# Optimization experiments

Hardware: AMD Instinct MI355X
Metric: run time of the kernel (lower is better)

## Reference

```python
import jax, jax.numpy as jnp
import numpy as np

DIM = 1024
HEADS = 16
HEAD_DIM = DIM // HEADS
MLP_HIDDEN = 4 * DIM
OUT_DIM = 1000
V_DIM = 1024
EPS = 1e-5
SCALE = DIM ** -0.5  # note: module scales by hidden_dim**-0.5, not head_dim**-0.5


def layer_norm(x, g, b):
    mu = jnp.mean(x, axis=-1, keepdims=True)
    var = jnp.mean(jnp.square(x - mu), axis=-1, keepdims=True)
    return (x - mu) * jax.lax.rsqrt(var + EPS) * g + b


def setup_inputs() -> dict:
    key = jax.random.key(0)
    ks = jax.random.split(key, 12)
    B, N = 4, 2048
    s = lambda fan_in: 1.0 / np.sqrt(fan_in)
    return {
        "x": jax.random.normal(ks[0], (B, N, DIM), jnp.float32),
        "value": jax.random.normal(ks[1], (B, N, V_DIM), jnp.float32),
        "wq": jax.random.normal(ks[2], (DIM, DIM), jnp.float32) * s(DIM),
        "wk": jax.random.normal(ks[3], (DIM, DIM), jnp.float32) * s(DIM),
        "wv": jax.random.normal(ks[4], (V_DIM, DIM), jnp.float32) * s(V_DIM),
        "w_ap": jax.random.normal(ks[5], (DIM, DIM), jnp.float32) * s(DIM),
        "b_ap": jnp.zeros((DIM,), jnp.float32),
        "g1": jnp.ones((DIM,), jnp.float32),
        "be1": jnp.zeros((DIM,), jnp.float32),
        "g2": jnp.ones((DIM,), jnp.float32),
        "be2": jnp.zeros((DIM,), jnp.float32),
        "w1": jax.random.normal(ks[6], (DIM, MLP_HIDDEN), jnp.float32) * s(DIM),
        "b1": jnp.zeros((MLP_HIDDEN,), jnp.float32),
        "w2": jax.random.normal(ks[7], (MLP_HIDDEN, DIM), jnp.float32) * s(MLP_HIDDEN),
        "b2": jnp.zeros((DIM,), jnp.float32),
        "w_out": jax.random.normal(ks[8], (DIM, OUT_DIM), jnp.float32) * s(DIM),
        "b_out": jnp.zeros((OUT_DIM,), jnp.float32),
    }


def reference(x, value, wq, wk, wv, w_ap, b_ap, g1, be1, g2, be2, w1, b1, w2, b2, w_out, b_out):
    B, N, C = x.shape
    xn = layer_norm(x, g1, be1)                      # [B,N,C]
    q = (xn @ wq).reshape(B, N, HEADS, HEAD_DIM)     # query and key both from norm1(x)
    k = (xn @ wk).reshape(B, N, HEADS, HEAD_DIM)
    v = (value @ wv).reshape(B, N, HEADS, HEAD_DIM)
    attn = jnp.einsum("bqhd,bkhd->bhqk", q, k) * SCALE
    attn = jax.nn.softmax(attn, axis=-1)
    o = jnp.einsum("bhqk,bkhd->bqhd", attn, v).reshape(B, N, C)
    x = x + (o @ w_ap + b_ap)                        # residual (dropouts are identity)
    h = jax.nn.gelu(layer_norm(x, g2, be2) @ w1 + b1, approximate=False)
    x = x + (h @ w2 + b2)
    return jax.nn.softmax(x @ w_out + b_out, axis=2)
```

## Files before the change

### kernel.cpp

```cpp
#include <hip/hip_runtime.h>
#include <math.h>

typedef unsigned short u16;
typedef unsigned int u32;
typedef __attribute__((ext_vector_type(4))) float f32x4;
typedef __attribute__((ext_vector_type(4))) int i32x4;
typedef __attribute__((ext_vector_type(8))) short short8;
typedef __attribute__((ext_vector_type(4))) unsigned short u16x4;
typedef __attribute__((ext_vector_type(4))) __fp16 f16x4;
typedef __attribute__((ext_vector_type(2))) __fp16 f16x2;

#define DEV __device__ __forceinline__

DEV u16 f2bf(float f) {
  unsigned u = __float_as_uint(f);
  u += 0x7FFFu + ((u >> 16) & 1u);
  return (u16)(u >> 16);
}

DEV float fexp2(float x) {
  float r;
  asm("v_exp_f32 %0, %1" : "=v"(r) : "v"(x));
  return r;
}

DEV void gload_lds16(const void* g, void* l) {
  __builtin_amdgcn_global_load_lds((const __attribute__((address_space(1))) void*)g,
                                   (__attribute__((address_space(3))) void*)l, 16, 0, 0);
}

enum { EPI_BF16 = 0, EPI_VT = 1, EPI_RESID_F32 = 2, EPI_GELU = 3, EPI_RESID_BF16 = 4, EPI_LOGITS = 5 };

__global__ void transpose_w(const float* __restrict__ in, u16* __restrict__ out,
                            int K, int Nsrc, int Nout) {
  __shared__ float tile[32][33];
  int k0 = blockIdx.x * 32, n0 = blockIdx.y * 32;
  int tx = threadIdx.x, ty = threadIdx.y;
#pragma unroll
  for (int i = 0; i < 4; ++i) {
    int k = k0 + ty + i * 8, n = n0 + tx;
    tile[ty + i * 8][tx] = (n < Nsrc) ? in[(size_t)k * Nsrc + n] : 0.0f;
  }
  __syncthreads();
#pragma unroll
  for (int i = 0; i < 4; ++i) {
    int n = n0 + ty + i * 8, k = k0 + tx;
    out[(size_t)n * K + k] = f2bf(tile[tx][ty + i * 8]);
  }
}

__global__ void convert_bf16(const float* __restrict__ in, u16* __restrict__ out, int n4) {
  int i = blockIdx.x * blockDim.x + threadIdx.x;
  int stride = gridDim.x * blockDim.x;
  for (int j = i; j < n4; j += stride) {
    f32x4 v = reinterpret_cast<const f32x4*>(in)[j];
    u16x4 o;
    o[0] = f2bf(v[0]); o[1] = f2bf(v[1]); o[2] = f2bf(v[2]); o[3] = f2bf(v[3]);
    reinterpret_cast<u16x4*>(out)[j] = o;
  }
}

DEV float blockReduceSum(float v) {
  __shared__ float red[4];
#pragma unroll
  for (int m = 32; m >= 1; m >>= 1) v += __shfl_xor(v, m);
  __syncthreads();
  if ((threadIdx.x & 63) == 0) red[threadIdx.x >> 6] = v;
  __syncthreads();
  return red[0] + red[1] + red[2] + red[3];
}

DEV float blockReduceMax(float v) {
  __shared__ float redm[4];
#pragma unroll
  for (int m = 32; m >= 1; m >>= 1) v = fmaxf(v, __shfl_xor(v, m));
  __syncthreads();
  if ((threadIdx.x & 63) == 0) redm[threadIdx.x >> 6] = v;
  __syncthreads();
  return fmaxf(fmaxf(redm[0], redm[1]), fmaxf(redm[2], redm[3]));
}

__global__ __launch_bounds__(256)
void layernorm_k(const float* __restrict__ x, const float* __restrict__ g,
                 const float* __restrict__ b, u16* __restrict__ out) {
  int row = blockIdx.x, t = threadIdx.x;
  const float* xr = x + (size_t)row * 1024;
  f32x4 v = *reinterpret_cast<const f32x4*>(xr + t * 4);
  float mu = blockReduceSum(v[0] + v[1] + v[2] + v[3]) * (1.0f / 1024.0f);
  f32x4 d;
  d[0] = v[0] - mu; d[1] = v[1] - mu; d[2] = v[2] - mu; d[3] = v[3] - mu;
  float var = blockReduceSum(d[0]*d[0] + d[1]*d[1] + d[2]*d[2] + d[3]*d[3]) * (1.0f / 1024.0f);
  float rstd = rsqrtf(var + 1e-5f);
  u16x4 o;
#pragma unroll
  for (int i = 0; i < 4; ++i) o[i] = f2bf(d[i] * rstd * g[t * 4 + i] + b[t * 4 + i]);
  *reinterpret_cast<u16x4*>(out + (size_t)row * 1024 + t * 4) = o;
}

__global__ __launch_bounds__(256)
void softmax_rows(float* __restrict__ io) {
  int row = blockIdx.x, t = threadIdx.x;
  float* p = io + (size_t)row * 1000;
  float v[4];
  float mx = -INFINITY;
#pragma unroll
  for (int i = 0; i < 4; ++i) {
    int c = t + i * 256;
    v[i] = (c < 1000) ? p[c] : -INFINITY;
    mx = fmaxf(mx, v[i]);
  }
  mx = blockReduceMax(mx);
  float s = 0.f;
#pragma unroll
  for (int i = 0; i < 4; ++i) {
    int c = t + i * 256;
    v[i] = (c < 1000) ? __expf(v[i] - mx) : 0.f;
    s += v[i];
  }
  s = blockReduceSum(s);
  float inv = 1.0f / s;
#pragma unroll
  for (int i = 0; i < 4; ++i) {
    int c = t + i * 256;
    if (c < 1000) p[c] = v[i] * inv;
  }
}

template<int EPI>
__global__ __launch_bounds__(256)
void gemm_bt(const u16* __restrict__ A, const u16* __restrict__ Bt,
             void* __restrict__ outp, const float* __restrict__ aux0,
             const float* __restrict__ aux1, int M, int N, int K, float scale) {
  __shared__ u16 As[128 * 64];
  __shared__ u16 Bs[128 * 64];
  const int t = threadIdx.x;
  const int lane = t & 63;
  const int w = t >> 6;
  const int wm = w >> 1, wn = w & 1;
  const int bm = blockIdx.y * 128, bn = blockIdx.x * 128;
  const int l15 = lane & 15, lg = lane >> 4;

  f32x4 acc[4][4] = {};

  const int r0 = t >> 3;
  const int sg = ((t & 7) ^ ((t >> 3) & 7)) * 8;

  for (int kt = 0; kt < K; kt += 64) {
    __syncthreads();
#pragma unroll
    for (int p = 0; p < 4; ++p) {
      int r = p * 32 + r0;
      gload_lds16(A  + (size_t)(bm + r) * K + kt + sg, &As[p * 2048 + t * 8]);
      gload_lds16(Bt + (size_t)(bn + r) * K + kt + sg, &Bs[p * 2048 + t * 8]);
    }
    __syncthreads();
#pragma unroll
    for (int ks = 0; ks < 2; ++ks) {
      short8 af[4], bfr[4];
#pragma unroll
      for (int i = 0; i < 4; ++i) {
        int rA = wm * 64 + i * 16 + l15;
        int sa = (lg + ks * 4) ^ (rA & 7);
        af[i] = *reinterpret_cast<const short8*>(&As[rA * 64 + sa * 8]);
        int rB = wn * 64 + i * 16 + l15;
        int sb = (lg + ks * 4) ^ (rB & 7);
        bfr[i] = *reinterpret_cast<const short8*>(&Bs[rB * 64 + sb * 8]);
      }
#pragma unroll
      for (int i = 0; i < 4; ++i)
#pragma unroll
        for (int j = 0; j < 4; ++j)
          acc[i][j] = __builtin_amdgcn_mfma_f32_16x16x32_bf16(af[i], bfr[j], acc[i][j], 0, 0, 0);
    }
  }

#pragma unroll
  for (int i = 0; i < 4; ++i)
#pragma unroll
    for (int j = 0; j < 4; ++j)
#pragma unroll
      for (int r = 0; r < 4; ++r) {
        int row = bm + wm * 64 + i * 16 + lg * 4 + r;
        int col = bn + wn * 64 + j * 16 + l15;
        float v = acc[i][j][r];
        if constexpr (EPI == EPI_BF16) {
          ((u16*)outp)[(size_t)row * N + col] = f2bf(v * scale);
        } else if constexpr (EPI == EPI_VT) {
          size_t idx = ((size_t)((row >> 11) * 16 + (col >> 6)) * 64 + (col & 63)) * 2048 + (row & 2047);
          __fp16 hv = (__fp16)v;
          ((u16*)outp)[idx] = *reinterpret_cast<u16*>(&hv);
        } else if constexpr (EPI == EPI_RESID_F32) {
          ((float*)outp)[(size_t)row * N + col] = v + aux0[col] + aux1[(size_t)row * N + col];
        } else if constexpr (EPI == EPI_GELU) {
          float tt = v + aux0[col];
          ((u16*)outp)[(size_t)row * N + col] = f2bf(0.5f * tt * (1.0f + erff(tt * 0.70710678118654752f)));
        } else if constexpr (EPI == EPI_RESID_BF16) {
          float tt = v + aux0[col] + aux1[(size_t)row * N + col];
          ((u16*)outp)[(size_t)row * N + col] = f2bf(tt);
        } else {
          if (col < 1000) ((float*)outp)[(size_t)row * 1000 + col] = v + aux0[col];
        }
      }
  (void)scale; (void)aux0; (void)aux1; (void)M;
}

__global__ __launch_bounds__(512)
void attn_flash(const u16* __restrict__ Qb, const u16* __restrict__ Kb,
                const u16* __restrict__ Vt, u16* __restrict__ Ob) {
  __shared__ u16 Ks[2][128 * 64];
  __shared__ u16 Vs[2][64 * 128];
  const int t = threadIdx.x;
  const int lane = t & 63, w = t >> 6;
  const int l15 = lane & 15, lg = lane >> 4;
  const int bh = blockIdx.x;
  const int b = bh >> 4, h = bh & 15;
  const int qrow0 = b * 2048 + blockIdx.y * 128 + w * 16;

  short8 qf[2];
#pragma unroll
  for (int ks = 0; ks < 2; ++ks)
    qf[ks] = *reinterpret_cast<const short8*>(Qb + (size_t)(qrow0 + l15) * 1024 + h * 64 + ks * 32 + lg * 8);

  f32x4 oacc[4] = {};
  float lpart = 0.f;

  const int sgK = ((t & 7) ^ ((t >> 3) & 7)) * 8;
  const int sgV = ((t & 15) ^ ((t >> 4) & 7)) * 8;
  const int tk8 = t * 8;

  auto STAGE = [&](int buf, int tt) {
    int kt = tt * 128;
#pragma unroll
    for (int p = 0; p < 2; ++p) {
      int rK = p * 64 + (t >> 3);
      gload_lds16(Kb + (size_t)(b * 2048 + kt + rK) * 1024 + h * 64 + sgK, &Ks[buf][p * 4096 + tk8]);
      int rV = p * 32 + (t >> 4);
      gload_lds16(Vt + ((size_t)bh * 64 + rV) * 2048 + kt + sgV, &Vs[buf][p * 4096 + tk8]);
    }
  };

  auto COMPUTE = [&](int buf) {
    f32x4 s[8];
#pragma unroll
    for (int cb = 0; cb < 8; ++cb) {
      s[cb] = f32x4{0.f, 0.f, 0.f, 0.f};
      int rK = cb * 16 + l15;
#pragma unroll
      for (int ks = 0; ks < 2; ++ks) {
        int sk = (lg + ks * 4) ^ (rK & 7);
        short8 kf = *reinterpret_cast<const short8*>(&Ks[buf][rK * 64 + sk * 8]);
        s[cb] = __builtin_amdgcn_mfma_f32_16x16x32_bf16(kf, qf[ks], s[cb], 0, 0, 0);
      }
    }

    const float L2E = 1.44269504088896f;
    const char* vbase = (const char*)&Vs[buf][0];
#pragma unroll
    for (int cb = 0; cb < 8; ++cb) {
      float e0 = fexp2(s[cb][0] * L2E), e1 = fexp2(s[cb][1] * L2E);
      float e2 = fexp2(s[cb][2] * L2E), e3 = fexp2(s[cb][3] * L2E);
      lpart += (e0 + e1) + (e2 + e3);
      f16x2 plo = __builtin_amdgcn_cvt_pkrtz(e0, e1);
      f16x2 phi = __builtin_amdgcn_cvt_pkrtz(e2, e3);
      f16x4 pf;
      pf[0] = plo[0]; pf[1] = plo[1]; pf[2] = phi[0]; pf[3] = phi[1];
#pragma unroll
      for (int db = 0; db < 4; ++db) {
        int d = db * 16 + l15;
        int boff = d * 256 + ((((2 * cb + (lg >> 1)) ^ (d & 7)) << 4) | ((lg & 1) << 3));
        f16x4 vf = *reinterpret_cast<const f16x4*>(vbase + boff);
        oacc[db] = __builtin_amdgcn_mfma_f32_16x16x16f16(pf, vf, oacc[db], 0, 0, 0);
      }
    }
  };

  STAGE(0, 0);
  __syncthreads();
#pragma unroll 1
  for (int i = 0; i < 8; ++i) {
    STAGE(1, 2 * i + 1);
    COMPUTE(0);
    __syncthreads();
    if (i < 7) STAGE(0, 2 * i + 2);
    COMPUTE(1);
    __syncthreads();
  }

  lpart += __shfl_xor(lpart, 16);
  lpart += __shfl_xor(lpart, 32);
  float inv = 1.0f / lpart;
  float invr[4];
#pragma unroll
  for (int r = 0; r < 4; ++r) invr[r] = __shfl(inv, lg * 4 + r);

#pragma unroll
  for (int db = 0; db < 4; ++db)
#pragma unroll
    for (int r = 0; r < 4; ++r) {
      int row = qrow0 + lg * 4 + r;
      int col = h * 64 + db * 16 + l15;
      Ob[(size_t)row * 1024 + col] = f2bf(oacc[db][r] * invr[r]);
    }
}

extern "C" void kernel_launch(void* const* d_in, const int* in_sizes, int n_in,
                              void* d_out, int out_size, void* d_ws, size_t ws_size,
                              hipStream_t stream) {
  (void)in_sizes; (void)n_in; (void)out_size; (void)ws_size;
  const float* x     = (const float*)d_in[0];
  const float* value = (const float*)d_in[1];
  const float* wq    = (const float*)d_in[2];
  const float* wk    = (const float*)d_in[3];
  const float* wv    = (const float*)d_in[4];
  const float* w_ap  = (const float*)d_in[5];
  const float* b_ap  = (const float*)d_in[6];
  const float* g1    = (const float*)d_in[7];
  const float* be1   = (const float*)d_in[8];
  const float* g2    = (const float*)d_in[9];
  const float* be2   = (const float*)d_in[10];
  const float* w1    = (const float*)d_in[11];
  const float* b1    = (const float*)d_in[12];
  const float* w2    = (const float*)d_in[13];
  const float* b2    = (const float*)d_in[14];
  const float* w_out = (const float*)d_in[15];
  const float* b_out = (const float*)d_in[16];

  char* ws = (char*)d_ws;
  u16* wqT   = (u16*)(ws + 0x0000000);
  u16* wkT   = (u16*)(ws + 0x0200000);
  u16* wvT   = (u16*)(ws + 0x0400000);
  u16* wapT  = (u16*)(ws + 0x0600000);
  u16* woutT = (u16*)(ws + 0x0800000);
  u16* w1T   = (u16*)(ws + 0x0A00000);
  u16* w2T   = (u16*)(ws + 0x1200000);
  u16* xn    = (u16*)(ws + 0x1A00000);
  u16* valb  = (u16*)(ws + 0x2A00000);
  u16* qb    = (u16*)(ws + 0x3A00000);
  u16* kb    = (u16*)(ws + 0x4A00000);
  u16* vT    = (u16*)(ws + 0x5A00000);
  u16* ob    = (u16*)(ws + 0x6A00000);
  float* x1  = (float*)(ws + 0x7A00000);
  u16* hb    = valb;
  u16* xn2   = xn;
  u16* x2b   = ob;

  dim3 tb(32, 8);
  transpose_w<<<dim3(32, 32),  tb, 0, stream>>>(wq,    wqT,   1024, 1024, 1024);
  transpose_w<<<dim3(32, 32),  tb, 0, stream>>>(wk,    wkT,   1024, 1024, 1024);
  transpose_w<<<dim3(32, 32),  tb, 0, stream>>>(wv,    wvT,   1024, 1024, 1024);
  transpose_w<<<dim3(32, 32),  tb, 0, stream>>>(w_ap,  wapT,  1024, 1024, 1024);
  transpose_w<<<dim3(32, 32),  tb, 0, stream>>>(w_out, woutT, 1024, 1000, 1024);
  transpose_w<<<dim3(32, 128), tb, 0, stream>>>(w1,    w1T,   1024, 4096, 4096);
  transpose_w<<<dim3(128, 32), tb, 0, stream>>>(w2,    w2T,   4096, 1024, 1024);

  convert_bf16<<<2048, 256, 0, stream>>>(value, valb, 2097152);
  layernorm_k<<<8192, 256, 0, stream>>>(x, g1, be1, xn);

  gemm_bt<EPI_BF16><<<dim3(8, 64), 256, 0, stream>>>(xn,   wqT, qb, nullptr, nullptr, 8192, 1024, 1024, 0.03125f);
  gemm_bt<EPI_BF16><<<dim3(8, 64), 256, 0, stream>>>(xn,   wkT, kb, nullptr, nullptr, 8192, 1024, 1024, 1.0f);
  gemm_bt<EPI_VT>  <<<dim3(8, 64), 256, 0, stream>>>(valb, wvT, vT, nullptr, nullptr, 8192, 1024, 1024, 1.0f);

  attn_flash<<<dim3(64, 16), 512, 0, stream>>>(qb, kb, vT, ob);

  gemm_bt<EPI_RESID_F32><<<dim3(8, 64),  256, 0, stream>>>(ob,  wapT, x1, b_ap, x, 8192, 1024, 1024, 1.0f);
  layernorm_k<<<8192, 256, 0, stream>>>(x1, g2, be2, xn2);
  gemm_bt<EPI_GELU>     <<<dim3(32, 64), 256, 0, stream>>>(xn2, w1T, hb, b1, nullptr, 8192, 4096, 1024, 1.0f);
  gemm_bt<EPI_RESID_BF16><<<dim3(8, 64), 256, 0, stream>>>(hb,  w2T, x2b, b2, x1, 8192, 1024, 4096, 1.0f);
  gemm_bt<EPI_LOGITS>   <<<dim3(8, 64),  256, 0, stream>>>(x2b, woutT, (float*)d_out, b_out, nullptr, 8192, 1024, 1024, 1.0f);
  softmax_rows<<<8192, 256, 0, stream>>>((float*)d_out);
}
```

Before: 497.9 us.

## Double-buffer GEMM LDS tiles, fuse Q/K projections, approximate GELU with tanh

The GEMM main loop now keeps two LDS buffers and issues the next tile's global-to-LDS loads before computing on the current tile, so load latency can overlap MFMA work with one barrier per iteration. The Q and K projections become a single GEMM writing an interleaved [N, 2048] buffer, which relies on wqT and wkT being adjacent in the workspace. Attention reads Q and K from that buffer. The exact erf GELU is replaced by a tanh approximation built on exp2, which changes numerics relative to the reference's exact GELU. Doubling the LDS footprint may reduce occupancy.

```diff
diff --git a/kernel.cpp b/kernel.cpp
--- a/kernel.cpp
+++ b/kernel.cpp
@@ -29,7 +29,7 @@
                                    (__attribute__((address_space(3))) void*)l, 16, 0, 0);
 }
 
-enum { EPI_BF16 = 0, EPI_VT = 1, EPI_RESID_F32 = 2, EPI_GELU = 3, EPI_RESID_BF16 = 4, EPI_LOGITS = 5 };
+enum { EPI_QK = 0, EPI_VT = 1, EPI_RESID_F32 = 2, EPI_GELU = 3, EPI_RESID_BF16 = 4, EPI_LOGITS = 5 };
 
 __global__ void transpose_w(const float* __restrict__ in, u16* __restrict__ out,
                             int K, int Nsrc, int Nout) {
@@ -131,8 +131,8 @@
 void gemm_bt(const u16* __restrict__ A, const u16* __restrict__ Bt,
              void* __restrict__ outp, const float* __restrict__ aux0,
              const float* __restrict__ aux1, int M, int N, int K, float scale) {
-  __shared__ u16 As[128 * 64];
-  __shared__ u16 Bs[128 * 64];
+  __shared__ u16 As[2][128 * 64];
+  __shared__ u16 Bs[2][128 * 64];
   const int t = threadIdx.x;
   const int lane = t & 63;
   const int w = t >> 6;
@@ -145,15 +145,16 @@
   const int r0 = t >> 3;
   const int sg = ((t & 7) ^ ((t >> 3) & 7)) * 8;
 
-  for (int kt = 0; kt < K; kt += 64) {
-    __syncthreads();
+  auto STAGE = [&](int buf, int kt) {
 #pragma unroll
     for (int p = 0; p < 4; ++p) {
       int r = p * 32 + r0;
-      gload_lds16(A  + (size_t)(bm + r) * K + kt + sg, &As[p * 2048 + t * 8]);
-      gload_lds16(Bt + (size_t)(bn + r) * K + kt + sg, &Bs[p * 2048 + t * 8]);
-    }
-    __syncthreads();
+      gload_lds16(A  + (size_t)(bm + r) * K + kt + sg, &As[buf][p * 2048 + t * 8]);
+      gload_lds16(Bt + (size_t)(bn + r) * K + kt + sg, &Bs[buf][p * 2048 + t * 8]);
+    }
+  };
+
+  auto COMPUTE = [&](int buf) {
 #pragma unroll
     for (int ks = 0; ks < 2; ++ks) {
       short8 af[4], bfr[4];
@@ -161,10 +162,10 @@
       for (int i = 0; i < 4; ++i) {
         int rA = wm * 64 + i * 16 + l15;
         int sa = (lg + ks * 4) ^ (rA & 7);
-        af[i] = *reinterpret_cast<const short8*>(&As[rA * 64 + sa * 8]);
+        af[i] = *reinterpret_cast<const short8*>(&As[buf][rA * 64 + sa * 8]);
         int rB = wn * 64 + i * 16 + l15;
         int sb = (lg + ks * 4) ^ (rB & 7);
-        bfr[i] = *reinterpret_cast<const short8*>(&Bs[rB * 64 + sb * 8]);
+        bfr[i] = *reinterpret_cast<const short8*>(&Bs[buf][rB * 64 + sb * 8]);
       }
 #pragma unroll
       for (int i = 0; i < 4; ++i)
@@ -172,7 +173,18 @@
         for (int j = 0; j < 4; ++j)
           acc[i][j] = __builtin_amdgcn_mfma_f32_16x16x32_bf16(af[i], bfr[j], acc[i][j], 0, 0, 0);
     }
-  }
+  };
+
+  const int nk = K >> 6;
+  STAGE(0, 0);
+  __syncthreads();
+#pragma unroll 1
+  for (int i = 0; i + 1 < nk; ++i) {
+    STAGE((i + 1) & 1, (i + 1) << 6);
+    COMPUTE(i & 1);
+    __syncthreads();
+  }
+  COMPUTE((nk - 1) & 1);
 
 #pragma unroll
   for (int i = 0; i < 4; ++i)
@@ -183,8 +195,9 @@
         int row = bm + wm * 64 + i * 16 + lg * 4 + r;
         int col = bn + wn * 64 + j * 16 + l15;
         float v = acc[i][j][r];
-        if constexpr (EPI == EPI_BF16) {
-          ((u16*)outp)[(size_t)row * N + col] = f2bf(v * scale);
+        if constexpr (EPI == EPI_QK) {
+          float sc = (col < 1024) ? 0.03125f : 1.0f;
+          ((u16*)outp)[(size_t)row * 2048 + col] = f2bf(v * sc);
         } else if constexpr (EPI == EPI_VT) {
           size_t idx = ((size_t)((row >> 11) * 16 + (col >> 6)) * 64 + (col & 63)) * 2048 + (row & 2047);
           __fp16 hv = (__fp16)v;
@@ -193,7 +206,10 @@
           ((float*)outp)[(size_t)row * N + col] = v + aux0[col] + aux1[(size_t)row * N + col];
         } else if constexpr (EPI == EPI_GELU) {
           float tt = v + aux0[col];
-          ((u16*)outp)[(size_t)row * N + col] = f2bf(0.5f * tt * (1.0f + erff(tt * 0.70710678118654752f)));
+          float u = tt * (0.7978845608f + 0.035677408f * tt * tt);
+          float e = fexp2(u * 2.8853900818f);
+          float gl = tt * (1.0f - 1.0f / (1.0f + e));
+          ((u16*)outp)[(size_t)row * N + col] = f2bf(gl);
         } else if constexpr (EPI == EPI_RESID_BF16) {
           float tt = v + aux0[col] + aux1[(size_t)row * N + col];
           ((u16*)outp)[(size_t)row * N + col] = f2bf(tt);
@@ -205,8 +221,8 @@
 }
 
 __global__ __launch_bounds__(512)
-void attn_flash(const u16* __restrict__ Qb, const u16* __restrict__ Kb,
-                const u16* __restrict__ Vt, u16* __restrict__ Ob) {
+void attn_flash(const u16* __restrict__ QKb, const u16* __restrict__ Vt,
+                u16* __restrict__ Ob) {
   __shared__ u16 Ks[2][128 * 64];
   __shared__ u16 Vs[2][64 * 128];
   const int t = threadIdx.x;
@@ -219,7 +235,7 @@
   short8 qf[2];
 #pragma unroll
   for (int ks = 0; ks < 2; ++ks)
-    qf[ks] = *reinterpret_cast<const short8*>(Qb + (size_t)(qrow0 + l15) * 1024 + h * 64 + ks * 32 + lg * 8);
+    qf[ks] = *reinterpret_cast<const short8*>(QKb + (size_t)(qrow0 + l15) * 2048 + h * 64 + ks * 32 + lg * 8);
 
   f32x4 oacc[4] = {};
   float lpart = 0.f;
@@ -233,7 +249,7 @@
 #pragma unroll
     for (int p = 0; p < 2; ++p) {
       int rK = p * 64 + (t >> 3);
-      gload_lds16(Kb + (size_t)(b * 2048 + kt + rK) * 1024 + h * 64 + sgK, &Ks[buf][p * 4096 + tk8]);
+      gload_lds16(QKb + (size_t)(b * 2048 + kt + rK) * 2048 + 1024 + h * 64 + sgK, &Ks[buf][p * 4096 + tk8]);
       int rV = p * 32 + (t >> 4);
       gload_lds16(Vt + ((size_t)bh * 64 + rV) * 2048 + kt + sgV, &Vs[buf][p * 4096 + tk8]);
     }
@@ -335,8 +351,7 @@
   u16* w2T   = (u16*)(ws + 0x1200000);
   u16* xn    = (u16*)(ws + 0x1A00000);
   u16* valb  = (u16*)(ws + 0x2A00000);
-  u16* qb    = (u16*)(ws + 0x3A00000);
-  u16* kb    = (u16*)(ws + 0x4A00000);
+  u16* qkb   = (u16*)(ws + 0x3A00000);
   u16* vT    = (u16*)(ws + 0x5A00000);
   u16* ob    = (u16*)(ws + 0x6A00000);
   float* x1  = (float*)(ws + 0x7A00000);
@@ -356,11 +371,10 @@
   convert_bf16<<<2048, 256, 0, stream>>>(value, valb, 2097152);
   layernorm_k<<<8192, 256, 0, stream>>>(x, g1, be1, xn);
 
-  gemm_bt<EPI_BF16><<<dim3(8, 64), 256, 0, stream>>>(xn,   wqT, qb, nullptr, nullptr, 8192, 1024, 1024, 0.03125f);
-  gemm_bt<EPI_BF16><<<dim3(8, 64), 256, 0, stream>>>(xn,   wkT, kb, nullptr, nullptr, 8192, 1024, 1024, 1.0f);
-  gemm_bt<EPI_VT>  <<<dim3(8, 64), 256, 0, stream>>>(valb, wvT, vT, nullptr, nullptr, 8192, 1024, 1024, 1.0f);
-
-  attn_flash<<<dim3(64, 16), 512, 0, stream>>>(qb, kb, vT, ob);
+  gemm_bt<EPI_QK><<<dim3(16, 64), 256, 0, stream>>>(xn,   wqT, qkb, nullptr, nullptr, 8192, 2048, 1024, 1.0f);
+  gemm_bt<EPI_VT><<<dim3(8, 64),  256, 0, stream>>>(valb, wvT, vT,  nullptr, nullptr, 8192, 1024, 1024, 1.0f);
+
+  attn_flash<<<dim3(64, 16), 512, 0, stream>>>(qkb, vT, ob);
 
   gemm_bt<EPI_RESID_F32><<<dim3(8, 64),  256, 0, stream>>>(ob,  wapT, x1, b_ap, x, 8192, 1024, 1024, 1.0f);
   layernorm_k<<<8192, 256, 0, stream>>>(x1, g2, be2, xn2);
```

New measurement: 480.4 us. 3.5% less time.
